# Optimization experiments

Hardware: AMD Instinct MI355X
Metric: run time of the kernel (lower is better)

The kernel has to match this reference:

```python
import jax, jax.numpy as jnp
import numpy as np

B, T, C, HS = 256, 256, 384, 64

def setup_inputs() -> dict:
    key = jax.random.key(0)
    k1, k2, k3, k4 = jax.random.split(key, 4)
    s = 1.0 / np.sqrt(C)  # Linear-like init scale
    return {
        "x": jax.random.normal(k1, (B, T, C), dtype=jnp.float32),
        "Wq": jax.random.normal(k2, (C, HS), dtype=jnp.float32) * s,
        "Wk": jax.random.normal(k3, (C, HS), dtype=jnp.float32) * s,
        "Wv": jax.random.normal(k4, (C, HS), dtype=jnp.float32) * s,
    }

def reference(x, Wq, Wk, Wv):
    # q,k,v: [B,T,HS]
    q = jnp.einsum("btc,ch->bth", x, Wq)
    k = jnp.einsum("btc,ch->bth", x, Wk)
    v = jnp.einsum("btc,ch->bth", x, Wv)
    scale = k.shape[-1] ** -0.5
    scores = jnp.einsum("bth,bsh->bts", q, k) * scale  # [B,T,T]
    causal = jnp.tril(jnp.ones((x.shape[1], x.shape[1]), dtype=bool))
    scores = jnp.where(causal, scores, -jnp.inf)
    attn = jax.nn.softmax(scores, axis=-1)
    # dropout omitted (eval mode / deterministic reference)
    return jnp.einsum("bts,bsh->bth", attn, v)
```

## Files before the change

### kernel.cpp

```cpp
#include <hip/hip_runtime.h>
#include <hip/hip_bf16.h>

#define NB 256
#define NT 256
#define NC 384
#define NH 64
#define NW 192
#define WT_ELEMS (NW * NC)

typedef short bf16x8 __attribute__((ext_vector_type(8)));
typedef float f32x4 __attribute__((ext_vector_type(4)));

__device__ __forceinline__ unsigned short f2bf(float f) {
  union { float f; unsigned int i; } c;
  c.f = f;
  const unsigned int r = c.i + 0x7fffu + ((c.i >> 16) & 1u);
  return (unsigned short)(r >> 16);
}

__device__ __forceinline__ unsigned short f2bf_hw(float f) {
  __hip_bfloat16 b = __float2bfloat16(f);
  return *reinterpret_cast<unsigned short*>(&b);
}

__global__ __launch_bounds__(256) void w_transpose_kernel(
    const float* __restrict__ Wq,
    const float* __restrict__ Wk,
    const float* __restrict__ Wv,
    unsigned short* __restrict__ Wt) {
  const int idx = blockIdx.x * 256 + threadIdx.x;
  if (idx >= WT_ELEMS) return;
  const int n = idx / NC, k = idx - n * NC;
  const float* W = (n < 64) ? Wq : (n < 128) ? Wk : Wv;
  Wt[idx] = f2bf(W[k * NH + (n & 63)]);
}

__global__ __launch_bounds__(512, 2) void fused_qkv_attn_kernel(
    const float* __restrict__ x,
    const unsigned short* __restrict__ Wt,
    float* __restrict__ out) {
  __shared__ __align__(16) unsigned char lds[118784];

  const int tid = threadIdx.x;
  const int w = tid >> 6;
  const int lane = tid & 63;
  const int l15 = lane & 15;
  const int lg = lane >> 4;
  const int b = blockIdx.x;
  const int row0 = b * NT;
  const int qt = (w < 4) ? w : 11 - w;
  const int wbase = qt * 32;

  f32x4 acc[2][12];
#pragma unroll
  for (int mi = 0; mi < 2; ++mi)
#pragma unroll
    for (int ni = 0; ni < 12; ++ni)
#pragma unroll
      for (int r = 0; r < 4; ++r) acc[mi][ni][r] = 0.f;

#define STAGE_X(buf, kt)                                                      \
  {                                                                           \
    _Pragma("unroll") for (int j = 0; j < 4; ++j) {                           \
      const int idx = j * 512 + tid;                                          \
      const int srow = idx >> 3, c = idx & 7;                                 \
      const float* src = x + (size_t)(row0 + srow) * NC + (kt)*32 +           \
                         ((c ^ (srow & 7)) << 2);                             \
      __builtin_amdgcn_global_load_lds(                                       \
          (const __attribute__((address_space(1))) void*)src,                 \
          (__attribute__((address_space(3))) void*)(lds + (buf)*32768 +       \
                                                    idx * 16),                \
          16, 0, 0);                                                          \
    }                                                                         \
  }

#define STAGE_W(buf, kt)                                                      \
  {                                                                           \
    _Pragma("unroll") for (int j = 0; j < 2; ++j) {                           \
      const int idx = j * 512 + tid;                                          \
      if (idx < 768) {                                                        \
        const int nrow = idx >> 2, c = idx & 3;                               \
        const unsigned short* src =                                           \
            Wt + (size_t)nrow * NC + (kt)*32 + ((c ^ (nrow & 3)) << 3);       \
        __builtin_amdgcn_global_load_lds(                                     \
            (const __attribute__((address_space(1))) void*)src,               \
            (__attribute__((address_space(3))) void*)(lds + 65536 +           \
                                                      (buf)*12288 + idx * 16),\
            16, 0, 0);                                                        \
      }                                                                       \
    }                                                                         \
  }

  STAGE_X(0, 0);
  STAGE_W(0, 0);
  __syncthreads();

  for (int kt = 0; kt < 12; ++kt) {
    const int cur = kt & 1;
    if (kt < 11) {
      STAGE_X(cur ^ 1, kt + 1);
      STAGE_W(cur ^ 1, kt + 1);
    }

    const float* Xc = reinterpret_cast<const float*>(lds + cur * 32768);
    const unsigned short* Wc =
        reinterpret_cast<const unsigned short*>(lds + 65536 + cur * 12288);

    bf16x8 afr[2];
#pragma unroll
    for (int mi = 0; mi < 2; ++mi) {
      const int rl = wbase + mi * 16 + l15;
      const int s0 = (lg * 2) ^ (rl & 7);
      const int s1 = (lg * 2 + 1) ^ (rl & 7);
      const float4 lo = *reinterpret_cast<const float4*>(Xc + rl * 32 + s0 * 4);
      const float4 hi = *reinterpret_cast<const float4*>(Xc + rl * 32 + s1 * 4);
      union { bf16x8 v; unsigned short u[8]; } au;
      au.u[0] = f2bf_hw(lo.x);
      au.u[1] = f2bf_hw(lo.y);
      au.u[2] = f2bf_hw(lo.z);
      au.u[3] = f2bf_hw(lo.w);
      au.u[4] = f2bf_hw(hi.x);
      au.u[5] = f2bf_hw(hi.y);
      au.u[6] = f2bf_hw(hi.z);
      au.u[7] = f2bf_hw(hi.w);
      afr[mi] = au.v;
    }
#pragma unroll
    for (int ni = 0; ni < 12; ++ni) {
      const int n = ni * 16 + l15;
      const int ch = lg ^ (n & 3);
      const bf16x8 bfr =
          *reinterpret_cast<const bf16x8*>(Wc + n * 32 + ch * 8);
      acc[0][ni] = __builtin_amdgcn_mfma_f32_16x16x32_bf16(
          afr[0], bfr, acc[0][ni], 0, 0, 0);
      acc[1][ni] = __builtin_amdgcn_mfma_f32_16x16x32_bf16(
          afr[1], bfr, acc[1][ni], 0, 0, 0);
    }
    __syncthreads();
  }

  unsigned short* Kls = reinterpret_cast<unsigned short*>(lds);
  unsigned short* Vtls = reinterpret_cast<unsigned short*>(lds + 32768);
  unsigned short* Qls = reinterpret_cast<unsigned short*>(lds + 65536);
  unsigned short* Pls = reinterpret_cast<unsigned short*>(lds + 98304);

#pragma unroll
  for (int mi = 0; mi < 2; ++mi)
#pragma unroll
    for (int ni = 0; ni < 12; ++ni) {
      const int n = ni * 16 + l15;
#pragma unroll
      for (int r = 0; r < 4; ++r) {
        const int srow = wbase + mi * 16 + lg * 4 + r;
        const unsigned short val = f2bf_hw(acc[mi][ni][r]);
        if (ni < 4) {
          Qls[srow * 64 + (n ^ ((srow & 7) << 3))] = val;
        } else if (ni < 8) {
          const int h = n - 64;
          Kls[srow * 64 + (h ^ ((srow & 7) << 3))] = val;
        } else {
          const int h = n - 128;
          Vtls[h * 256 + (srow ^ ((h & 7) << 3))] = val;
        }
      }
    }
  __syncthreads();

  const int q0 = wbase;
  bf16x8 a_q[2][2];
#pragma unroll
  for (int mi = 0; mi < 2; ++mi)
#pragma unroll
    for (int ks = 0; ks < 2; ++ks) {
      const int srow = q0 + mi * 16 + l15;
      a_q[mi][ks] = *reinterpret_cast<const bf16x8*>(
          Qls + srow * 64 + ((ks * 32 + lg * 8) ^ ((srow & 7) << 3)));
    }

  f32x4 o[2][4];
  float mrun[2][4], lrun[2][4];
#pragma unroll
  for (int mi = 0; mi < 2; ++mi)
#pragma unroll
    for (int r = 0; r < 4; ++r) {
      mrun[mi][r] = -3.0e38f;
      lrun[mi][r] = 0.f;
#pragma unroll
      for (int hi = 0; hi < 4; ++hi) o[mi][hi][r] = 0.f;
    }

  unsigned short* Pw = Pls + w * 1280;

  for (int j = 0; j <= qt; ++j) {
    f32x4 s_acc[2][2];
#pragma unroll
    for (int mi = 0; mi < 2; ++mi)
#pragma unroll
      for (int si = 0; si < 2; ++si)
#pragma unroll
        for (int r = 0; r < 4; ++r) s_acc[mi][si][r] = 0.f;

#pragma unroll
    for (int ks = 0; ks < 2; ++ks) {
      bf16x8 bk[2];
#pragma unroll
      for (int si = 0; si < 2; ++si) {
        const int srow = j * 32 + si * 16 + l15;
        const int kel = ks * 32 + lg * 8;
        bk[si] = *reinterpret_cast<const bf16x8*>(
            Kls + srow * 64 + (kel ^ ((srow & 7) << 3)));
      }
#pragma unroll
      for (int mi = 0; mi < 2; ++mi)
#pragma unroll
        for (int si = 0; si < 2; ++si)
          s_acc[mi][si] = __builtin_amdgcn_mfma_f32_16x16x32_bf16(
              a_q[mi][ks], bk[si], s_acc[mi][si], 0, 0, 0);
    }

    const bool diag = (j == qt);
#pragma unroll
    for (int mi = 0; mi < 2; ++mi) {
#pragma unroll
      for (int r = 0; r < 4; ++r) {
        const int mloc = mi * 16 + lg * 4 + r;
        float v0 = s_acc[mi][0][r] * 0.125f;
        float v1 = s_acc[mi][1][r] * 0.125f;
        if (diag) {
          if (l15 > mloc) v0 = -3.0e38f;
          if (16 + l15 > mloc) v1 = -3.0e38f;
        }
        float pm = fmaxf(v0, v1);
        pm = fmaxf(pm, __shfl_xor(pm, 1, 16));
        pm = fmaxf(pm, __shfl_xor(pm, 2, 16));
        pm = fmaxf(pm, __shfl_xor(pm, 4, 16));
        pm = fmaxf(pm, __shfl_xor(pm, 8, 16));
        const float mnew = fmaxf(mrun[mi][r], pm);
        const float alpha = __expf(mrun[mi][r] - mnew);
        mrun[mi][r] = mnew;
        const float p0 = __expf(v0 - mnew);
        const float p1 = __expf(v1 - mnew);
        float ps = p0 + p1;
        ps += __shfl_xor(ps, 1, 16);
        ps += __shfl_xor(ps, 2, 16);
        ps += __shfl_xor(ps, 4, 16);
        ps += __shfl_xor(ps, 8, 16);
        lrun[mi][r] = lrun[mi][r] * alpha + ps;
#pragma unroll
        for (int hi = 0; hi < 4; ++hi) o[mi][hi][r] *= alpha;
        Pw[mloc * 40 + l15] = f2bf(p0);
        Pw[mloc * 40 + 16 + l15] = f2bf(p1);
      }
    }

    bf16x8 pa[2];
#pragma unroll
    for (int mt = 0; mt < 2; ++mt)
      pa[mt] = *reinterpret_cast<const bf16x8*>(
          Pw + (mt * 16 + l15) * 40 + lg * 8);
#pragma unroll
    for (int hi = 0; hi < 4; ++hi) {
      const int h = hi * 16 + l15;
      const int sel = j * 32 + lg * 8;
      const bf16x8 bv = *reinterpret_cast<const bf16x8*>(
          Vtls + h * 256 + (sel ^ ((h & 7) << 3)));
#pragma unroll
      for (int mt = 0; mt < 2; ++mt)
        o[mt][hi] = __builtin_amdgcn_mfma_f32_16x16x32_bf16(
            pa[mt], bv, o[mt][hi], 0, 0, 0);
    }
  }

  float* og = out + ((size_t)b * NT + q0) * NH;
#pragma unroll
  for (int mi = 0; mi < 2; ++mi)
#pragma unroll
    for (int r = 0; r < 4; ++r) {
      const float inv = 1.f / lrun[mi][r];
      const int m = mi * 16 + lg * 4 + r;
#pragma unroll
      for (int hi = 0; hi < 4; ++hi)
        og[m * 64 + hi * 16 + l15] = o[mi][hi][r] * inv;
    }
}

extern "C" void kernel_launch(void* const* d_in, const int* in_sizes, int n_in,
                              void* d_out, int out_size, void* d_ws,
                              size_t ws_size, hipStream_t stream) {
  const float* x  = (const float*)d_in[0];
  const float* Wq = (const float*)d_in[1];
  const float* Wk = (const float*)d_in[2];
  const float* Wv = (const float*)d_in[3];
  unsigned short* Wt = (unsigned short*)d_ws;
  float* out = (float*)d_out;

  w_transpose_kernel<<<dim3((WT_ELEMS + 255) / 256), dim3(256), 0, stream>>>(
      Wq, Wk, Wv, Wt);
  fused_qkv_attn_kernel<<<dim3(NB), dim3(512), 0, stream>>>(x, Wt, out);
}
```

Before: 46.73 us.

## Triple-buffer QKV projection staging with explicit vmcnt waits

Replaces the double-buffered x/W staging loop of the QKV projection with a three-stage ring buffer, prefetching two tiles ahead. It swaps the full __syncthreads for partial vmcnt waits plus raw barriers, so global-to-LDS loads stay in flight while the MFMAs run. The W loads become branch-free: threads beyond 768 redundantly reload an existing chunk, which keeps the per-stage load count uniform for the vmcnt accounting. LDS use grows, and the hand-counted waits are fragile if the number of issued loads changes.

Measured after the change: 42.81 us. 1.09x faster.

```diff
diff --git a/kernel.cpp b/kernel.cpp
--- a/kernel.cpp
+++ b/kernel.cpp
@@ -35,11 +35,14 @@
   Wt[idx] = f2bf(W[k * NH + (n & 63)]);
 }
 
+#define XB 32768
+#define WB 12288
+#define XTOT 98304
 __global__ __launch_bounds__(512, 2) void fused_qkv_attn_kernel(
     const float* __restrict__ x,
     const unsigned short* __restrict__ Wt,
     float* __restrict__ out) {
-  __shared__ __align__(16) unsigned char lds[118784];
+  __shared__ __align__(16) unsigned char lds[XTOT + 3 * WB];
 
   const int tid = threadIdx.x;
   const int w = tid >> 6;
@@ -59,7 +62,7 @@
 #pragma unroll
       for (int r = 0; r < 4; ++r) acc[mi][ni][r] = 0.f;
 
-#define STAGE_X(buf, kt)                                                      \
+#define STAGE(buf, kt)                                                        \
   {                                                                           \
     _Pragma("unroll") for (int j = 0; j < 4; ++j) {                           \
       const int idx = j * 512 + tid;                                          \
@@ -68,81 +71,84 @@
                          ((c ^ (srow & 7)) << 2);                             \
       __builtin_amdgcn_global_load_lds(                                       \
           (const __attribute__((address_space(1))) void*)src,                 \
-          (__attribute__((address_space(3))) void*)(lds + (buf)*32768 +       \
+          (__attribute__((address_space(3))) void*)(lds + (buf)*XB +          \
+                                                    idx * 16),                \
+          16, 0, 0);                                                          \
+    }                                                                         \
+    _Pragma("unroll") for (int j = 0; j < 2; ++j) {                           \
+      const int raw = j * 512 + tid;                                          \
+      const int idx = (raw < 768) ? raw : raw - 256;                          \
+      const int nrow = idx >> 2, c = idx & 3;                                 \
+      const unsigned short* src =                                             \
+          Wt + (size_t)nrow * NC + (kt)*32 + ((c ^ (nrow & 3)) << 3);         \
+      __builtin_amdgcn_global_load_lds(                                       \
+          (const __attribute__((address_space(1))) void*)src,                 \
+          (__attribute__((address_space(3))) void*)(lds + XTOT + (buf)*WB +   \
                                                     idx * 16),                \
           16, 0, 0);                                                          \
     }                                                                         \
   }
 
-#define STAGE_W(buf, kt)                                                      \
+#define COMPUTE(buf)                                                          \
   {                                                                           \
-    _Pragma("unroll") for (int j = 0; j < 2; ++j) {                           \
-      const int idx = j * 512 + tid;                                          \
-      if (idx < 768) {                                                        \
-        const int nrow = idx >> 2, c = idx & 3;                               \
-        const unsigned short* src =                                           \
-            Wt + (size_t)nrow * NC + (kt)*32 + ((c ^ (nrow & 3)) << 3);       \
-        __builtin_amdgcn_global_load_lds(                                     \
-            (const __attribute__((address_space(1))) void*)src,               \
-            (__attribute__((address_space(3))) void*)(lds + 65536 +           \
-                                                      (buf)*12288 + idx * 16),\
-            16, 0, 0);                                                        \
-      }                                                                       \
+    const float* Xc = reinterpret_cast<const float*>(lds + (buf)*XB);         \
+    const unsigned short* Wc =                                                \
+        reinterpret_cast<const unsigned short*>(lds + XTOT + (buf)*WB);       \
+    bf16x8 afr[2];                                                            \
+    _Pragma("unroll") for (int mi = 0; mi < 2; ++mi) {                        \
+      const int rl = wbase + mi * 16 + l15;                                   \
+      const int s0 = (lg * 2) ^ (rl & 7);                                     \
+      const int s1 = (lg * 2 + 1) ^ (rl & 7);                                 \
+      const float4 lo =                                                       \
+          *reinterpret_cast<const float4*>(Xc + rl * 32 + s0 * 4);            \
+      const float4 hi =                                                       \
+          *reinterpret_cast<const float4*>(Xc + rl * 32 + s1 * 4);            \
+      union { bf16x8 v; unsigned short u[8]; } au;                            \
+      au.u[0] = f2bf_hw(lo.x); au.u[1] = f2bf_hw(lo.y);                       \
+      au.u[2] = f2bf_hw(lo.z); au.u[3] = f2bf_hw(lo.w);                       \
+      au.u[4] = f2bf_hw(hi.x); au.u[5] = f2bf_hw(hi.y);                       \
+      au.u[6] = f2bf_hw(hi.z); au.u[7] = f2bf_hw(hi.w);                       \
+      afr[mi] = au.v;                                                         \
+    }                                                                         \
+    _Pragma("unroll") for (int ni = 0; ni < 12; ++ni) {                       \
+      const int n = ni * 16 + l15;                                            \
+      const int ch = lg ^ (n & 3);                                            \
+      const bf16x8 bfr =                                                      \
+          *reinterpret_cast<const bf16x8*>(Wc + n * 32 + ch * 8);             \
+      acc[0][ni] = __builtin_amdgcn_mfma_f32_16x16x32_bf16(                   \
+          afr[0], bfr, acc[0][ni], 0, 0, 0);                                  \
+      acc[1][ni] = __builtin_amdgcn_mfma_f32_16x16x32_bf16(                   \
+          afr[1], bfr, acc[1][ni], 0, 0, 0);                                  \
     }                                                                         \
   }
 
-  STAGE_X(0, 0);
-  STAGE_W(0, 0);
+  STAGE(0, 0);
+  STAGE(1, 1);
+  STAGE(2, 2);
+
+  int bufc = 0;
+  for (int t = 0; t < 10; ++t) {
+    asm volatile("s_waitcnt vmcnt(12)" ::: "memory");
+    __builtin_amdgcn_s_barrier();
+    COMPUTE(bufc);
+    asm volatile("s_waitcnt lgkmcnt(0)" ::: "memory");
+    __builtin_amdgcn_s_barrier();
+    if (t < 9) STAGE(bufc, t + 3);
+    bufc = (bufc == 2) ? 0 : bufc + 1;
+  }
+  asm volatile("s_waitcnt vmcnt(6)" ::: "memory");
+  __builtin_amdgcn_s_barrier();
+  COMPUTE(1);
+  asm volatile("s_waitcnt vmcnt(0)" ::: "memory");
+  __builtin_amdgcn_s_barrier();
+  COMPUTE(2);
+
   __syncthreads();
-
-  for (int kt = 0; kt < 12; ++kt) {
-    const int cur = kt & 1;
-    if (kt < 11) {
-      STAGE_X(cur ^ 1, kt + 1);
-      STAGE_W(cur ^ 1, kt + 1);
-    }
-
-    const float* Xc = reinterpret_cast<const float*>(lds + cur * 32768);
-    const unsigned short* Wc =
-        reinterpret_cast<const unsigned short*>(lds + 65536 + cur * 12288);
-
-    bf16x8 afr[2];
-#pragma unroll
-    for (int mi = 0; mi < 2; ++mi) {
-      const int rl = wbase + mi * 16 + l15;
-      const int s0 = (lg * 2) ^ (rl & 7);
-      const int s1 = (lg * 2 + 1) ^ (rl & 7);
-      const float4 lo = *reinterpret_cast<const float4*>(Xc + rl * 32 + s0 * 4);
-      const float4 hi = *reinterpret_cast<const float4*>(Xc + rl * 32 + s1 * 4);
-      union { bf16x8 v; unsigned short u[8]; } au;
-      au.u[0] = f2bf_hw(lo.x);
-      au.u[1] = f2bf_hw(lo.y);
-      au.u[2] = f2bf_hw(lo.z);
-      au.u[3] = f2bf_hw(lo.w);
-      au.u[4] = f2bf_hw(hi.x);
-      au.u[5] = f2bf_hw(hi.y);
-      au.u[6] = f2bf_hw(hi.z);
-      au.u[7] = f2bf_hw(hi.w);
-      afr[mi] = au.v;
-    }
-#pragma unroll
-    for (int ni = 0; ni < 12; ++ni) {
-      const int n = ni * 16 + l15;
-      const int ch = lg ^ (n & 3);
-      const bf16x8 bfr =
-          *reinterpret_cast<const bf16x8*>(Wc + n * 32 + ch * 8);
-      acc[0][ni] = __builtin_amdgcn_mfma_f32_16x16x32_bf16(
-          afr[0], bfr, acc[0][ni], 0, 0, 0);
-      acc[1][ni] = __builtin_amdgcn_mfma_f32_16x16x32_bf16(
-          afr[1], bfr, acc[1][ni], 0, 0, 0);
-    }
-    __syncthreads();
-  }
 
   unsigned short* Kls = reinterpret_cast<unsigned short*>(lds);
   unsigned short* Vtls = reinterpret_cast<unsigned short*>(lds + 32768);
   unsigned short* Qls = reinterpret_cast<unsigned short*>(lds + 65536);
-  unsigned short* Pls = reinterpret_cast<unsigned short*>(lds + 98304);
+  unsigned short* Pls = reinterpret_cast<unsigned short*>(lds + XTOT);
 
 #pragma unroll
   for (int mi = 0; mi < 2; ++mi)
```

## Stage QKV projection through registers with bf16 LDS and padded layout

Applied to the files above, without the earlier changes.

Replaces the direct global-to-LDS async loads of fp32 x and bf16 W with a register-staged two-deep prefetch: global loads land in registers two steps ahead, x is converted to bf16 once on write, and tiles are stored in a padded (stride 40) LDS layout instead of XOR swizzling. This halves the LDS footprint and bandwidth for x and removes the repeated per-wave fp32-to-bf16 conversion at fragment load time. The cost is extra VGPRs for the staged data on top of 96 accumulator registers, plus explicit waits that may serialize global latency differently than the async path.

Result: faster. 43.00 us (-8.0%).

```diff
diff --git a/kernel.cpp b/kernel.cpp
--- a/kernel.cpp
+++ b/kernel.cpp
@@ -59,85 +59,105 @@
 #pragma unroll
       for (int r = 0; r < 4; ++r) acc[mi][ni][r] = 0.f;
 
-#define STAGE_X(buf, kt)                                                      \
-  {                                                                           \
-    _Pragma("unroll") for (int j = 0; j < 4; ++j) {                           \
-      const int idx = j * 512 + tid;                                          \
-      const int srow = idx >> 3, c = idx & 7;                                 \
-      const float* src = x + (size_t)(row0 + srow) * NC + (kt)*32 +           \
-                         ((c ^ (srow & 7)) << 2);                             \
-      __builtin_amdgcn_global_load_lds(                                       \
-          (const __attribute__((address_space(1))) void*)src,                 \
-          (__attribute__((address_space(3))) void*)(lds + (buf)*32768 +       \
-                                                    idx * 16),                \
-          16, 0, 0);                                                          \
+  int xrow[4], xcol[4];
+#pragma unroll
+  for (int j = 0; j < 4; ++j) {
+    const int idx = j * 512 + tid;
+    xrow[j] = idx >> 3;
+    xcol[j] = idx & 7;
+  }
+  int wnr[2], wcc[2];
+  {
+    const int i0 = tid;
+    const int raw = 512 + tid;
+    const int i1 = (raw < 768) ? raw : raw - 256;
+    wnr[0] = i0 >> 2; wcc[0] = i0 & 3;
+    wnr[1] = i1 >> 2; wcc[1] = i1 & 3;
+  }
+
+  float4 xA0, xA1, xA2, xA3, xB0, xB1, xB2, xB3;
+  bf16x8 wA0, wA1, wB0, wB1;
+
+#define XL(BUF) reinterpret_cast<unsigned short*>(lds + (BUF)*20480)
+#define WL(BUF) reinterpret_cast<unsigned short*>(lds + 40960 + (BUF)*15360)
+
+#define RLOAD(S, KT)                                                          \
+  do {                                                                        \
+    x##S##0 = *reinterpret_cast<const float4*>(                               \
+        x + (size_t)(row0 + xrow[0]) * NC + (KT)*32 + xcol[0] * 4);           \
+    x##S##1 = *reinterpret_cast<const float4*>(                               \
+        x + (size_t)(row0 + xrow[1]) * NC + (KT)*32 + xcol[1] * 4);           \
+    x##S##2 = *reinterpret_cast<const float4*>(                               \
+        x + (size_t)(row0 + xrow[2]) * NC + (KT)*32 + xcol[2] * 4);           \
+    x##S##3 = *reinterpret_cast<const float4*>(                               \
+        x + (size_t)(row0 + xrow[3]) * NC + (KT)*32 + xcol[3] * 4);           \
+    w##S##0 = *reinterpret_cast<const bf16x8*>(                               \
+        Wt + (size_t)wnr[0] * NC + (KT)*32 + wcc[0] * 8);                     \
+    w##S##1 = *reinterpret_cast<const bf16x8*>(                               \
+        Wt + (size_t)wnr[1] * NC + (KT)*32 + wcc[1] * 8);                     \
+  } while (0)
+
+#define WRX(BUF, V, J)                                                        \
+  do {                                                                        \
+    ushort4 t_;                                                               \
+    t_.x = f2bf_hw((V).x); t_.y = f2bf_hw((V).y);                             \
+    t_.z = f2bf_hw((V).z); t_.w = f2bf_hw((V).w);                             \
+    *reinterpret_cast<ushort4*>(XL(BUF) + xrow[J] * 40 + xcol[J] * 4) = t_;   \
+  } while (0)
+
+#define WRITE(BUF, S)                                                         \
+  do {                                                                        \
+    WRX(BUF, x##S##0, 0); WRX(BUF, x##S##1, 1);                               \
+    WRX(BUF, x##S##2, 2); WRX(BUF, x##S##3, 3);                               \
+    *reinterpret_cast<bf16x8*>(WL(BUF) + wnr[0] * 40 + wcc[0] * 8) = w##S##0; \
+    *reinterpret_cast<bf16x8*>(WL(BUF) + wnr[1] * 40 + wcc[1] * 8) = w##S##1; \
+  } while (0)
+
+#define COMPUTE(BUF)                                                          \
+  do {                                                                        \
+    const unsigned short* Xc = XL(BUF);                                       \
+    const unsigned short* Wc = WL(BUF);                                       \
+    const bf16x8 afr0 = *reinterpret_cast<const bf16x8*>(                     \
+        Xc + (wbase + l15) * 40 + lg * 8);                                    \
+    const bf16x8 afr1 = *reinterpret_cast<const bf16x8*>(                     \
+        Xc + (wbase + 16 + l15) * 40 + lg * 8);                               \
+    _Pragma("unroll") for (int ni = 0; ni < 12; ++ni) {                       \
+      const bf16x8 bfr = *reinterpret_cast<const bf16x8*>(                    \
+          Wc + (ni * 16 + l15) * 40 + lg * 8);                                \
+      acc[0][ni] = __builtin_amdgcn_mfma_f32_16x16x32_bf16(                   \
+          afr0, bfr, acc[0][ni], 0, 0, 0);                                    \
+      acc[1][ni] = __builtin_amdgcn_mfma_f32_16x16x32_bf16(                   \
+          afr1, bfr, acc[1][ni], 0, 0, 0);                                    \
     }                                                                         \
-  }
-
-#define STAGE_W(buf, kt)                                                      \
-  {                                                                           \
-    _Pragma("unroll") for (int j = 0; j < 2; ++j) {                           \
-      const int idx = j * 512 + tid;                                          \
-      if (idx < 768) {                                                        \
-        const int nrow = idx >> 2, c = idx & 3;                               \
-        const unsigned short* src =                                           \
-            Wt + (size_t)nrow * NC + (kt)*32 + ((c ^ (nrow & 3)) << 3);       \
-        __builtin_amdgcn_global_load_lds(                                     \
-            (const __attribute__((address_space(1))) void*)src,               \
-            (__attribute__((address_space(3))) void*)(lds + 65536 +           \
-                                                      (buf)*12288 + idx * 16),\
-            16, 0, 0);                                                        \
-      }                                                                       \
-    }                                                                         \
-  }
-
-  STAGE_X(0, 0);
-  STAGE_W(0, 0);
-  __syncthreads();
-
-  for (int kt = 0; kt < 12; ++kt) {
-    const int cur = kt & 1;
-    if (kt < 11) {
-      STAGE_X(cur ^ 1, kt + 1);
-      STAGE_W(cur ^ 1, kt + 1);
-    }
-
-    const float* Xc = reinterpret_cast<const float*>(lds + cur * 32768);
-    const unsigned short* Wc =
-        reinterpret_cast<const unsigned short*>(lds + 65536 + cur * 12288);
-
-    bf16x8 afr[2];
-#pragma unroll
-    for (int mi = 0; mi < 2; ++mi) {
-      const int rl = wbase + mi * 16 + l15;
-      const int s0 = (lg * 2) ^ (rl & 7);
-      const int s1 = (lg * 2 + 1) ^ (rl & 7);
-      const float4 lo = *reinterpret_cast<const float4*>(Xc + rl * 32 + s0 * 4);
-      const float4 hi = *reinterpret_cast<const float4*>(Xc + rl * 32 + s1 * 4);
-      union { bf16x8 v; unsigned short u[8]; } au;
-      au.u[0] = f2bf_hw(lo.x);
-      au.u[1] = f2bf_hw(lo.y);
-      au.u[2] = f2bf_hw(lo.z);
-      au.u[3] = f2bf_hw(lo.w);
-      au.u[4] = f2bf_hw(hi.x);
-      au.u[5] = f2bf_hw(hi.y);
-      au.u[6] = f2bf_hw(hi.z);
-      au.u[7] = f2bf_hw(hi.w);
-      afr[mi] = au.v;
-    }
-#pragma unroll
-    for (int ni = 0; ni < 12; ++ni) {
-      const int n = ni * 16 + l15;
-      const int ch = lg ^ (n & 3);
-      const bf16x8 bfr =
-          *reinterpret_cast<const bf16x8*>(Wc + n * 32 + ch * 8);
-      acc[0][ni] = __builtin_amdgcn_mfma_f32_16x16x32_bf16(
-          afr[0], bfr, acc[0][ni], 0, 0, 0);
-      acc[1][ni] = __builtin_amdgcn_mfma_f32_16x16x32_bf16(
-          afr[1], bfr, acc[1][ni], 0, 0, 0);
-    }
-    __syncthreads();
-  }
+  } while (0)
+
+#define STEP(T, CUR, NXT, L2, W1)                                             \
+  do {                                                                        \
+    if (L2) RLOAD(CUR, (T) + 2);                                              \
+    if (W1) WRITE(((T) + 1) & 1, NXT);                                        \
+    COMPUTE((T)&1);                                                           \
+    asm volatile("s_waitcnt lgkmcnt(0)" ::: "memory");                        \
+    __builtin_amdgcn_s_barrier();                                             \
+  } while (0)
+
+  RLOAD(A, 0);
+  RLOAD(B, 1);
+  WRITE(0, A);
+  asm volatile("s_waitcnt lgkmcnt(0)" ::: "memory");
+  __builtin_amdgcn_s_barrier();
+
+  STEP(0, A, B, 1, 1);
+  STEP(1, B, A, 1, 1);
+  STEP(2, A, B, 1, 1);
+  STEP(3, B, A, 1, 1);
+  STEP(4, A, B, 1, 1);
+  STEP(5, B, A, 1, 1);
+  STEP(6, A, B, 1, 1);
+  STEP(7, B, A, 1, 1);
+  STEP(8, A, B, 1, 1);
+  STEP(9, B, A, 1, 1);
+  STEP(10, A, B, 0, 1);
+  STEP(11, B, A, 0, 0);
 
   unsigned short* Kls = reinterpret_cast<unsigned short*>(lds);
   unsigned short* Vtls = reinterpret_cast<unsigned short*>(lds + 32768);
```

## Load QKV projection operands directly from global into MFMA fragments, drop LDS staging

Applied to the files above, without the earlier changes.

Replaces the double-buffered global-to-LDS staging of x and transposed weights in the QKV projection with direct per-lane global loads into registers. The weight prep kernel now writes weights pre-arranged in MFMA fragment order, so each lane reads one contiguous 16-byte fragment per tile. This removes LDS traffic and the per-iteration __syncthreads. In exchange, x reads become strided 32-byte accesses per lane with no explicit prefetch, and the shared weights are re-read from L2 by every wave, so latency hiding depends on unroll and occupancy.

After: 44.94 us. 1.04x faster.

```diff
diff --git a/kernel.cpp b/kernel.cpp
--- a/kernel.cpp
+++ b/kernel.cpp
@@ -23,21 +23,36 @@
   return *reinterpret_cast<unsigned short*>(&b);
 }
 
-__global__ __launch_bounds__(256) void w_transpose_kernel(
+__device__ __forceinline__ bf16x8 cvt8(float4 lo, float4 hi) {
+  union { bf16x8 v; unsigned short u[8]; } au;
+  au.u[0] = f2bf_hw(lo.x); au.u[1] = f2bf_hw(lo.y);
+  au.u[2] = f2bf_hw(lo.z); au.u[3] = f2bf_hw(lo.w);
+  au.u[4] = f2bf_hw(hi.x); au.u[5] = f2bf_hw(hi.y);
+  au.u[6] = f2bf_hw(hi.z); au.u[7] = f2bf_hw(hi.w);
+  return au.v;
+}
+
+__global__ __launch_bounds__(256) void w_prep_kernel(
     const float* __restrict__ Wq,
     const float* __restrict__ Wk,
     const float* __restrict__ Wv,
-    unsigned short* __restrict__ Wt) {
-  const int idx = blockIdx.x * 256 + threadIdx.x;
-  if (idx >= WT_ELEMS) return;
-  const int n = idx / NC, k = idx - n * NC;
+    unsigned short* __restrict__ Wt2) {
+  const int o = blockIdx.x * 256 + threadIdx.x;
+  if (o >= WT_ELEMS) return;
+  const int j = o & 7;
+  const int lane = (o >> 3) & 63;
+  const int fi = o >> 9;
+  const int ni = fi % 12;
+  const int kt = fi / 12;
+  const int n = ni * 16 + (lane & 15);
+  const int k = kt * 32 + ((lane >> 4) << 3) + j;
   const float* W = (n < 64) ? Wq : (n < 128) ? Wk : Wv;
-  Wt[idx] = f2bf(W[k * NH + (n & 63)]);
+  Wt2[o] = f2bf(W[k * NH + (n & 63)]);
 }
 
 __global__ __launch_bounds__(512, 2) void fused_qkv_attn_kernel(
     const float* __restrict__ x,
-    const unsigned short* __restrict__ Wt,
+    const unsigned short* __restrict__ Wt2,
     float* __restrict__ out) {
   __shared__ __align__(16) unsigned char lds[118784];
 
@@ -59,84 +74,27 @@
 #pragma unroll
       for (int r = 0; r < 4; ++r) acc[mi][ni][r] = 0.f;
 
-#define STAGE_X(buf, kt)                                                      \
-  {                                                                           \
-    _Pragma("unroll") for (int j = 0; j < 4; ++j) {                           \
-      const int idx = j * 512 + tid;                                          \
-      const int srow = idx >> 3, c = idx & 7;                                 \
-      const float* src = x + (size_t)(row0 + srow) * NC + (kt)*32 +           \
-                         ((c ^ (srow & 7)) << 2);                             \
-      __builtin_amdgcn_global_load_lds(                                       \
-          (const __attribute__((address_space(1))) void*)src,                 \
-          (__attribute__((address_space(3))) void*)(lds + (buf)*32768 +       \
-                                                    idx * 16),                \
-          16, 0, 0);                                                          \
-    }                                                                         \
-  }
-
-#define STAGE_W(buf, kt)                                                      \
-  {                                                                           \
-    _Pragma("unroll") for (int j = 0; j < 2; ++j) {                           \
-      const int idx = j * 512 + tid;                                          \
-      if (idx < 768) {                                                        \
-        const int nrow = idx >> 2, c = idx & 3;                               \
-        const unsigned short* src =                                           \
-            Wt + (size_t)nrow * NC + (kt)*32 + ((c ^ (nrow & 3)) << 3);       \
-        __builtin_amdgcn_global_load_lds(                                     \
-            (const __attribute__((address_space(1))) void*)src,               \
-            (__attribute__((address_space(3))) void*)(lds + 65536 +           \
-                                                      (buf)*12288 + idx * 16),\
-            16, 0, 0);                                                        \
-      }                                                                       \
-    }                                                                         \
-  }
-
-  STAGE_X(0, 0);
-  STAGE_W(0, 0);
-  __syncthreads();
-
+  const float* xa0 = x + (size_t)(row0 + wbase + l15) * NC + lg * 8;
+  const float* xa1 = xa0 + (size_t)16 * NC;
+  const unsigned short* wfrag = Wt2 + lane * 8;
+
+#pragma unroll 2
   for (int kt = 0; kt < 12; ++kt) {
-    const int cur = kt & 1;
-    if (kt < 11) {
-      STAGE_X(cur ^ 1, kt + 1);
-      STAGE_W(cur ^ 1, kt + 1);
-    }
-
-    const float* Xc = reinterpret_cast<const float*>(lds + cur * 32768);
-    const unsigned short* Wc =
-        reinterpret_cast<const unsigned short*>(lds + 65536 + cur * 12288);
-
-    bf16x8 afr[2];
-#pragma unroll
-    for (int mi = 0; mi < 2; ++mi) {
-      const int rl = wbase + mi * 16 + l15;
-      const int s0 = (lg * 2) ^ (rl & 7);
-      const int s1 = (lg * 2 + 1) ^ (rl & 7);
-      const float4 lo = *reinterpret_cast<const float4*>(Xc + rl * 32 + s0 * 4);
-      const float4 hi = *reinterpret_cast<const float4*>(Xc + rl * 32 + s1 * 4);
-      union { bf16x8 v; unsigned short u[8]; } au;
-      au.u[0] = f2bf_hw(lo.x);
-      au.u[1] = f2bf_hw(lo.y);
-      au.u[2] = f2bf_hw(lo.z);
-      au.u[3] = f2bf_hw(lo.w);
-      au.u[4] = f2bf_hw(hi.x);
-      au.u[5] = f2bf_hw(hi.y);
-      au.u[6] = f2bf_hw(hi.z);
-      au.u[7] = f2bf_hw(hi.w);
-      afr[mi] = au.v;
-    }
+    const float4 a0lo = *reinterpret_cast<const float4*>(xa0 + kt * 32);
+    const float4 a0hi = *reinterpret_cast<const float4*>(xa0 + kt * 32 + 4);
+    const float4 a1lo = *reinterpret_cast<const float4*>(xa1 + kt * 32);
+    const float4 a1hi = *reinterpret_cast<const float4*>(xa1 + kt * 32 + 4);
+    const bf16x8 afr0 = cvt8(a0lo, a0hi);
+    const bf16x8 afr1 = cvt8(a1lo, a1hi);
 #pragma unroll
     for (int ni = 0; ni < 12; ++ni) {
-      const int n = ni * 16 + l15;
-      const int ch = lg ^ (n & 3);
-      const bf16x8 bfr =
-          *reinterpret_cast<const bf16x8*>(Wc + n * 32 + ch * 8);
+      const bf16x8 bfr = *reinterpret_cast<const bf16x8*>(
+          wfrag + (size_t)(kt * 12 + ni) * 512);
       acc[0][ni] = __builtin_amdgcn_mfma_f32_16x16x32_bf16(
-          afr[0], bfr, acc[0][ni], 0, 0, 0);
+          afr0, bfr, acc[0][ni], 0, 0, 0);
       acc[1][ni] = __builtin_amdgcn_mfma_f32_16x16x32_bf16(
-          afr[1], bfr, acc[1][ni], 0, 0, 0);
-    }
-    __syncthreads();
+          afr1, bfr, acc[1][ni], 0, 0, 0);
+    }
   }
 
   unsigned short* Kls = reinterpret_cast<unsigned short*>(lds);
@@ -291,10 +249,10 @@
   const float* Wq = (const float*)d_in[1];
   const float* Wk = (const float*)d_in[2];
   const float* Wv = (const float*)d_in[3];
-  unsigned short* Wt = (unsigned short*)d_ws;
+  unsigned short* Wt2 = (unsigned short*)d_ws;
   float* out = (float*)d_out;
 
-  w_transpose_kernel<<<dim3((WT_ELEMS + 255) / 256), dim3(256), 0, stream>>>(
-      Wq, Wk, Wv, Wt);
-  fused_qkv_attn_kernel<<<dim3(NB), dim3(512), 0, stream>>>(x, Wt, out);
-}
+  w_prep_kernel<<<dim3((WT_ELEMS + 255) / 256), dim3(256), 0, stream>>>(
+      Wq, Wk, Wv, Wt2);
+  fused_qkv_attn_kernel<<<dim3(NB), dim3(512), 0, stream>>>(x, Wt2, out);
+}
```
